# Kernel optimization log

Hardware: AMD Instinct MI355X
Metric: run time of the kernel (lower is better)

The kernel has to match this reference:

```python
import jax, jax.numpy as jnp
import numpy as np

N = 20000      # num_nodes
E = 320000     # num_edges (avg degree 16)
HID = 256      # hid_dim
H = 4          # attention heads
D = HID // H   # per-head dim (concat heads -> HID)
L = 2          # nGAT_layer
OUT = 12       # out_dim / pred_len (decoder steps)
NEG_SLOPE = 0.2


def setup_inputs() -> dict:
    key = jax.random.key(0)
    ks = jax.random.split(key, 16)
    s = 0.05
    nrm = lambda k, shape: jax.random.normal(k, shape, jnp.float32) * s
    return dict(
        x=nrm(ks[0], (N, HID)),
        edge_index=jax.random.randint(ks[1], (2, E), 0, N, dtype=jnp.int32),
        # GATv2Conv params per layer (stacked over L layers)
        gat_w_src=nrm(ks[2], (L, HID, H * D)),
        gat_w_dst=nrm(ks[3], (L, HID, H * D)),
        gat_att=nrm(ks[4], (L, H, D)),
        gat_bias=nrm(ks[5], (L, H * D)),
        # decoder_mlp: Linear(1 + HID -> HID)
        mlp_w=nrm(ks[6], (HID, 1 + HID)),
        mlp_b=nrm(ks[7], (HID,)),
        # nn.LSTM (1 layer, input HID, hidden HID), torch gate order i,f,g,o
        lstm_w_ih=nrm(ks[8], (4 * HID, HID)),
        lstm_w_hh=nrm(ks[9], (4 * HID, HID)),
        lstm_b_ih=nrm(ks[10], (4 * HID,)),
        lstm_b_hh=nrm(ks[11], (4 * HID,)),
        # decoder_init_proj: Linear(HID -> 1); decoder_output_proj: Linear(HID -> 1)
        init_w=nrm(ks[12], (1, HID)),
        init_b=nrm(ks[13], (1,)),
        out_w=nrm(ks[14], (1, HID)),
        out_b=nrm(ks[15], (1,)),
    )


def _gatv2_layer(x, src, dst, w_src, w_dst, att, bias):
    n = x.shape[0]
    xl = (x @ w_src).reshape(n, H, D)   # source-side projection
    xr = (x @ w_dst).reshape(n, H, D)   # destination-side projection
    # GATv2: e_ij = a^T LeakyReLU(Wl x_j + Wr x_i)
    e = jax.nn.leaky_relu(xl[src] + xr[dst], NEG_SLOPE)        # [E,H,D]
    logits = jnp.einsum('ehd,hd->eh', e, att)                   # [E,H]
    # edge softmax over incoming edges of each destination node
    m = jax.ops.segment_max(logits, dst, num_segments=n)        # [N,H]
    ex = jnp.exp(logits - m[dst])
    denom = jax.ops.segment_sum(ex, dst, num_segments=n)
    alpha = ex / denom[dst]                                     # [E,H]
    out = jax.ops.segment_sum(xl[src] * alpha[:, :, None], dst, num_segments=n)
    return out.reshape(n, H * D) + bias


def reference(x, edge_index, gat_w_src, gat_w_dst, gat_att, gat_bias,
              mlp_w, mlp_b, lstm_w_ih, lstm_w_hh, lstm_b_ih, lstm_b_hh,
              init_w, init_b, out_w, out_b):
    src, dst = edge_index[0], edge_index[1]
    # stacked GAT blocks: GATv2Conv + ELU (element == 2)
    for l in range(L):
        x = _gatv2_layer(x, src, dst, gat_w_src[l], gat_w_dst[l], gat_att[l], gat_bias[l])
        x = jax.nn.elu(x)
    # recurrent LSTM decoder, batch = nodes, seq step by step
    ctx = x                      # encoder_context
    h = x                        # h_0 = x (num_layers = 1)
    c = jnp.zeros_like(x)        # c_0 = 0
    prev = x @ init_w.T + init_b  # [N,1]
    outs = []
    for _ in range(OUT):
        dec_in = jnp.concatenate([prev, ctx], axis=1) @ mlp_w.T + mlp_b  # [N,HID]
        gates = dec_in @ lstm_w_ih.T + lstm_b_ih + h @ lstm_w_hh.T + lstm_b_hh
        i_g, f_g, g_g, o_g = jnp.split(gates, 4, axis=1)
        i_g = jax.nn.sigmoid(i_g)
        f_g = jax.nn.sigmoid(f_g)
        o_g = jax.nn.sigmoid(o_g)
        g_g = jnp.tanh(g_g)
        c = f_g * c + i_g * g_g
        h = o_g * jnp.tanh(c)
        prev = h @ out_w.T + out_b  # [N,1]
        outs.append(prev)
    return jnp.concatenate(outs, axis=1)  # [N, OUT]
```

## Files before the change

kernel.cpp:

```cpp
#include <hip/hip_runtime.h>
#include <hip/hip_bf16.h>

#define NN 20000
#define NE 320000
#define TOUT 12
#define DEGMAX 96
#define MR 80
#define NBLK 250
#define NCHL 14
#define NCHG 6

typedef __bf16 bf16x8 __attribute__((ext_vector_type(8)));
typedef float float4v __attribute__((ext_vector_type(4)));

#define LD8(p) (*(const bf16x8*)(p))
#define MFMA16(a,b,c) __builtin_amdgcn_mfma_f32_16x16x32_bf16((a),(b),(c),0,0,0)

__device__ __forceinline__ float bf2f(const __hip_bfloat16 v){ return __bfloat162float(v); }
__device__ __forceinline__ __hip_bfloat16 f2bf(float v){ return __float2bfloat16(v); }
__device__ __forceinline__ float sigmoidr_(float x){ return __builtin_amdgcn_rcpf(1.f + __expf(-x)); }
__device__ __forceinline__ float tanhr_(float x){ return 1.f - 2.f*__builtin_amdgcn_rcpf(__expf(2.f*x) + 1.f); }
__device__ __forceinline__ float rdf(const void* p, int i, int f32){
  return f32 ? ((const float*)p)[i] : __bfloat162float(((const __hip_bfloat16*)p)[i]);
}

__global__ void k_detect(const void* xraw, int* flag){
  __shared__ int cnt;
  if(threadIdx.x == 0) cnt = 0;
  __syncthreads();
  const unsigned* w = (const unsigned*)xraw;
  int local = 0;
  for(int i = threadIdx.x; i < 4096; i += 256){
    unsigned b = (w[i] >> 8) & 0x7F;
    if(b >= 0x33 && b <= 0x3F) local++;
  }
  atomicAdd(&cnt, local);
  __syncthreads();
  if(threadIdx.x == 0) *flag = (cnt > 2048) ? 0 : 1;
}

__global__ void k_fail(float* out, int n){
  int i = blockIdx.x*256 + threadIdx.x;
  if(i < n) out[i] = 256.0f;
}

__global__ void k_count(const int* __restrict__ dst, int* __restrict__ deg){
  int e = blockIdx.x*256 + threadIdx.x;
  if(e < NE){
    unsigned d = (unsigned)dst[e];
    if(d < NN) atomicAdd(&deg[d], 1);
  }
}

__global__ void k_scan(const int* __restrict__ deg, int* __restrict__ offp, int* __restrict__ cursor){
  __shared__ int part[256];
  __shared__ int excl[257];
  const int CH = (NN + 255)/256;
  int tid = threadIdx.x;
  int lo = tid*CH;
  int hi = lo + CH; if(hi > NN) hi = NN;
  int s = 0;
  for(int i=lo;i<hi;i++) s += deg[i];
  part[tid] = s;
// ... 36 lines not shown
    wdstT[tid] = f2bf(rdf(w_dst, l*65536 + i*256 + o, f));
  }
  if(tid < 262144){
    whhp[tid] = f2bf(rdf(w_hh, tid, f));
    wihb[tid] = f2bf(rdf(wih, tid, f));
  }
  if(tid < 65536){
    int k = tid >> 8, j = tid & 255;
    mlpT[tid] = f2bf(rdf(mlp_w, j*257 + 1 + k, f));
  }
}

__global__ void k_prep_ub(const void* __restrict__ wih, const void* __restrict__ mlp_w,
                          const void* __restrict__ mlp_b,
                          const void* __restrict__ b_ih, const void* __restrict__ b_hh,
                          const void* __restrict__ att, const void* __restrict__ gbias,
                          const void* __restrict__ init_w, const void* __restrict__ init_b,
                          const void* __restrict__ out_w, const void* __restrict__ out_b,
                          const int* __restrict__ flag,
                          float* __restrict__ u, float* __restrict__ bc,
                          float* __restrict__ attf, float* __restrict__ gbiasf,
                          float* __restrict__ initwf, float* __restrict__ outwf,
                          float* __restrict__ sc){
  __shared__ float su[256], sb[256];
  int g = blockIdx.x, j = threadIdx.x, f = *flag;
  float w = rdf(wih, g*256 + j, f);
  su[j] = w * rdf(mlp_w, j*257, f);
  sb[j] = w * rdf(mlp_b, j, f);
  if(g < 2){
    int i = g*256 + j;
    attf[i] = rdf(att, i, f);
    gbiasf[i] = rdf(gbias, i, f);
  }
  if(g == 0){
    initwf[j] = rdf(init_w, j, f);
    outwf[j]  = rdf(out_w, j, f);
    if(j == 0){ sc[0] = rdf(init_b, 0, f); sc[1] = rdf(out_b, 0, f); }
  }
  __syncthreads();
  for(int s=128; s>0; s>>=1){
    if(j < s){ su[j] += su[j+s]; sb[j] += sb[j+s]; }
    __syncthreads();
  }
  if(j == 0){ u[g] = su[0]; bc[g] = sb[0] + rdf(b_ih, g, f) + rdf(b_hh, g, f); }
}

__global__ void k_fold(const __hip_bfloat16* __restrict__ whh_pl,
                       const float* __restrict__ u_vec, const float* __restrict__ outwf,
                       __hip_bfloat16* __restrict__ whh2_pl){
  int i = blockIdx.x*256 + threadIdx.x;
  whh2_pl[i] = f2bf(bf2f(whh_pl[i]) + u_vec[i >> 8]*outwf[i & 255]);
}

__global__ void k_pack(const __hip_bfloat16* __restrict__ Wpl, const __hip_bfloat16* __restrict__ W2pl,
                       const __hip_bfloat16* __restrict__ Wcpl,
                       __hip_bfloat16* __restrict__ WhhP, __hip_bfloat16* __restrict__ Whh2P,
                       __hip_bfloat16* __restrict__ WcP){
  int idx = blockIdx.x*256 + threadIdx.x;
  if(idx >= 32768) return;
  int cs = idx >> 12;
  int kslot = (idx >> 9) & 7;
  int nt = (idx >> 6) & 7;
  int lane = idx & 63;
  int l16 = lane & 15, quad = lane >> 4;
  int brow = (nt>>1)*256 + cs*32 + (nt&1)*16 + l16;
  int srcofs = brow*256 + kslot*32 + quad*8;
  int dst = idx*8;
  *(bf16x8*)(WhhP + dst)  = LD8(Wpl + srcofs);
  *(bf16x8*)(Whh2P + dst) = LD8(W2pl + srcofs);
  *(bf16x8*)(WcP + dst)   = LD8(Wcpl + srcofs);
}

__global__ void k_pack2(const __hip_bfloat16* __restrict__ wsrcT,
                        const __hip_bfloat16* __restrict__ wdstT,
                        __hip_bfloat16* __restrict__ wprojP){
  int idx = blockIdx.x*256 + threadIdx.x;
  if(idx >= 32768) return;
  int m = idx >> 13;
  int fi = idx & 8191;
  int l = m >> 1, role = m & 1;
  int kidx = fi >> 10;
  int nt = (fi >> 6) & 15;
  int lane = fi & 63;
  int l16 = lane & 15, quad = lane >> 4;
  const __hip_bfloat16* src = (role ? wdstT : wsrcT) + l*65536;
  int srcofs = (nt*16 + l16)*256 + kidx*32 + quad*8;
  *(bf16x8*)(wprojP + (size_t)m*65536 + fi*8) = LD8(src + srcofs);
}

__global__ __launch_bounds__(256) void k_gemm_nt_bf(const __hip_bfloat16* __restrict__ A,
                                                    const __hip_bfloat16* __restrict__ B,
                                                    __hip_bfloat16* __restrict__ Cb, int M){
  int wave = threadIdx.x >> 6;
  int lane = threadIdx.x & 63;
  int l16 = lane & 15, quad = lane >> 4, quad8 = quad*8;
  int mBase = blockIdx.x*64 + wave*16;
  int nBase = blockIdx.y*64;
  int arow = mBase + l16; if(arow >= M) arow = M-1;
  const __hip_bfloat16* aptr = A + (size_t)arow*256 + quad8;
  float4v acc[4];
  #pragma unroll
  for(int nt=0;nt<4;nt++){ acc[nt][0]=0.f; acc[nt][1]=0.f; acc[nt][2]=0.f; acc[nt][3]=0.f; }
  for(int k0=0;k0<256;k0+=32){
    bf16x8 a = LD8(aptr + k0);
    #pragma unroll
    for(int nt=0;nt<4;nt++){
      const __hip_bfloat16* bptr = B + (size_t)(nBase + nt*16 + l16)*256 + k0 + quad8;
      acc[nt] = MFMA16(a, LD8(bptr), acc[nt]);
    }
  }
  #pragma unroll
  for(int nt=0;nt<4;nt++){
    int col = nBase + nt*16 + l16;
    #pragma unroll
    for(int r=0;r<4;r++){
      int row = mBase + quad*4 + r;
      if(row < M) Cb[(size_t)row*256 + col] = f2bf(acc[nt][r]);
    }
  }
// ... 94 lines not shown
      for(int j=0;j<4;j++){
        int d = h*64 + j*16 + li;
        float v = bf2f(pl[d]) + prl[h*4+j];
        v = (v > 0.f) ? v : 0.2f*v;
        p += v * attl[h*4+j];
      }
      part[h] = p;
    }
    #pragma unroll
    for(int h=0;h<4;h++){
      part[h] += __shfl_xor(part[h], 1, 64);
      part[h] += __shfl_xor(part[h], 2, 64);
      part[h] += __shfl_xor(part[h], 4, 64);
      part[h] += __shfl_xor(part[h], 8, 64);
    }
    if(li == 0 && valid){
      #pragma unroll
      for(int h=0;h<4;h++) slog[e*4+h] = part[h];
    }
  }
  __syncthreads();
  {
    int hh = tid >> 6;
    int li64 = tid & 63;
    float m = -1e30f;
    for(int i=li64; i<deg; i+=64) m = fmaxf(m, slog[i*4+hh]);
    #pragma unroll
    for(int s=1; s<64; s<<=1) m = fmaxf(m, __shfl_xor(m, s, 64));
    float den = 0.f;
    for(int i=li64; i<deg; i+=64) den += __expf(slog[i*4+hh] - m);
    #pragma unroll
    for(int s=1; s<64; s<<=1) den += __shfl_xor(den, s, 64);
    float inv = (den > 0.f) ? 1.f/den : 0.f;
    for(int i=li64; i<deg; i+=64) slog[i*4+hh] = __expf(slog[i*4+hh] - m)*inv;
  }
  __syncthreads();
  int d = tid, hd = d>>6;
  float acc = 0.f;
  for(int i=0;i<deg;i++) acc += slog[i*4+hd] * bf2f(Q[(size_t)ssrc[i]*256 + d]);
  acc += gbiasf[d];
  acc = (acc > 0.f) ? acc : (__expf(acc) - 1.f);
  P[(size_t)node*256 + d] = f2bf(acc);
}

__global__ __launch_bounds__(512, 1) void k_lstm80(const __hip_bfloat16* __restrict__ ctx,
                                                   const __hip_bfloat16* __restrict__ WcP,
                                                   const __hip_bfloat16* __restrict__ WhhP,
                                                   const __hip_bfloat16* __restrict__ Whh2P,
                                                   const float* __restrict__ u_vec,
                                                   const float* __restrict__ bc_vec,
                                                   const float* __restrict__ initwf,
                                                   const float* __restrict__ outwf,
                                                   const float* __restrict__ sc,
                                                   __hip_bfloat16* __restrict__ gxg,
                                                   float* __restrict__ out){
  __shared__ __hip_bfloat16 sgx[NCHL*4096];
  __shared__ __hip_bfloat16 sh[MR*264];
  __shared__ float spartw[MR*8];
  __shared__ float sprev0[MR];
  float* spart = (float*)sgx;
  int tid = threadIdx.x;
  int mBase = blockIdx.x*MR;
  int cs = tid>>6, lane = tid&63, l16 = lane&15, quad = lane>>4, quad8 = quad*8;
  int phase = (blockIdx.x >> 3) & 7;
  __hip_bfloat16* gxb = gxg + (size_t)blockIdx.x*(NCHG*4096);
  #pragma unroll
  for(int p=0;p<3;p++){
    int r = p*32 + (tid >> 4);
    if(r < MR){
      int c0 = (tid & 15)*16;
      const __hip_bfloat16* srcp = ctx + (size_t)(mBase + r)*256 + c0;
      *(bf16x8*)(&sh[r*264 + c0])     = LD8(srcp);
      *(bf16x8*)(&sh[r*264 + c0 + 8]) = LD8(srcp + 8);
    }
  }
  __syncthreads();
  #pragma unroll
  for(int p=0;p<3;p++){
    int r = p*32 + (tid >> 4);
    int c0 = (tid & 15)*16;
    float part = 0.f;
    if(r < MR){
      #pragma unroll
      for(int j=0;j<16;j++) part += bf2f(sh[r*264 + c0 + j]) * initwf[c0 + j];
    }
    spart[tid] = part;
    __syncthreads();
    if(tid < 32 && p*32 + tid < MR){
      float s = 0.f;
      #pragma unroll
      for(int j=0;j<16;j++) s += spart[tid*16 + j];
      sprev0[p*32 + tid] = s + sc[0];
    }
    __syncthreads();
  }
  float owreg[2];
  #pragma unroll
  for(int tc=0;tc<2;tc++) owreg[tc] = outwf[cs*32 + tc*16 + l16];
  float outb = sc[1];
  {
    float bcl[8];
    #pragma unroll
    for(int g=0;g<4;g++)
      #pragma unroll
      for(int tc=0;tc<2;tc++)
        bcl[g*2+tc] = bc_vec[g*256 + cs*32 + tc*16 + l16]
                    + u_vec[g*256 + cs*32 + tc*16 + l16]*outb;
    float4v acc[40];
    #pragma unroll
    for(int nt=0;nt<40;nt++){ acc[nt][0]=0.f; acc[nt][1]=0.f; acc[nt][2]=0.f; acc[nt][3]=0.f; }
    #pragma unroll 2
    for(int ki=0;ki<8;ki++){
      int kidx = (ki + phase) & 7;
      int k0 = kidx*32;
      bf16x8 a0 = *(const bf16x8*)(&sh[l16*264 + k0 + quad8]);
      bf16x8 a1 = *(const bf16x8*)(&sh[(16 + l16)*264 + k0 + quad8]);
      bf16x8 a2 = *(const bf16x8*)(&sh[(32 + l16)*264 + k0 + quad8]);
      bf16x8 a3 = *(const bf16x8*)(&sh[(48 + l16)*264 + k0 + quad8]);
      bf16x8 a4 = *(const bf16x8*)(&sh[(64 + l16)*264 + k0 + quad8]);
      const __hip_bfloat16* bbase = WcP + (((cs<<3) + kidx)<<12) + (lane<<3);
      #pragma unroll
      for(int nt=0;nt<8;nt++){
        bf16x8 b = LD8(bbase + (nt<<9));
        acc[nt]    = MFMA16(a0, b, acc[nt]);
        acc[8+nt]  = MFMA16(a1, b, acc[8+nt]);
        acc[16+nt] = MFMA16(a2, b, acc[16+nt]);
        acc[24+nt] = MFMA16(a3, b, acc[24+nt]);
        acc[32+nt] = MFMA16(a4, b, acc[32+nt]);
      }
    }
    #pragma unroll
    for(int rt=0;rt<5;rt++)
      #pragma unroll
      for(int tc=0;tc<2;tc++)
        #pragma unroll
        for(int half=0;half<2;half++){
          bf16x8 v;
          #pragma unroll
          for(int rr=0;rr<2;rr++)
            #pragma unroll
            for(int g=0;g<4;g++){
              int r = half*2 + rr;
              v[rr*4+g] = (__bf16)f2bf(acc[rt*8 + g*2 + tc][r] + bcl[g*2+tc]);
            }
          int cp = (rt*2+tc)*2 + half;
          if(cp < NCHL) *(bf16x8*)(&sgx[cp*4096 + tid*8]) = v;
          else          *(bf16x8*)(gxb + (cp-NCHL)*4096 + tid*8) = v;
        }
  }
  __syncthreads();
  float creg[40];
  #pragma unroll
  for(int i=0;i<40;i++) creg[i] = 0.f;
  #pragma unroll 1
  for(int step=0; step<TOUT; step++){
    const __hip_bfloat16* W = (step == 0) ? WhhP : Whh2P;
    float4v acc[40];
    #pragma unroll
    for(int nt=0;nt<40;nt++){ acc[nt][0]=0.f; acc[nt][1]=0.f; acc[nt][2]=0.f; acc[nt][3]=0.f; }
    #pragma unroll 2
    for(int ki=0;ki<8;ki++){
      int kidx = (ki + phase) & 7;
      int k0 = kidx*32;
      bf16x8 a0 = *(const bf16x8*)(&sh[l16*264 + k0 + quad8]);
      bf16x8 a1 = *(const bf16x8*)(&sh[(16 + l16)*264 + k0 + quad8]);
      bf16x8 a2 = *(const bf16x8*)(&sh[(32 + l16)*264 + k0 + quad8]);
      bf16x8 a3 = *(const bf16x8*)(&sh[(48 + l16)*264 + k0 + quad8]);
      bf16x8 a4 = *(const bf16x8*)(&sh[(64 + l16)*264 + k0 + quad8]);
      const __hip_bfloat16* bbase = W + (((cs<<3) + kidx)<<12) + (lane<<3);
      #pragma unroll
      for(int nt=0;nt<8;nt++){
        bf16x8 b = LD8(bbase + (nt<<9));
        acc[nt]    = MFMA16(a0, b, acc[nt]);
        acc[8+nt]  = MFMA16(a1, b, acc[8+nt]);
        acc[16+nt] = MFMA16(a2, b, acc[16+nt]);
        acc[24+nt] = MFMA16(a3, b, acc[24+nt]);
        acc[32+nt] = MFMA16(a4, b, acc[32+nt]);
      }
    }
    __syncthreads();
    #pragma unroll
    for(int ri=0; ri<5; ri++){
      const int rt = 4 - ri;
      float hsum[4];
      hsum[0]=0.f; hsum[1]=0.f; hsum[2]=0.f; hsum[3]=0.f;
      #pragma unroll
      for(int tc=0;tc<2;tc++){
        int col = cs*32 + tc*16 + l16;
        const int cpb = (rt*2+tc)*2;
        bf16x8 ga, gb;
        if(cpb < NCHL)   ga = *(const bf16x8*)(&sgx[cpb*4096 + tid*8]);
        else             ga = LD8(gxb + (cpb-NCHL)*4096 + tid*8);
        if(cpb+1 < NCHL) gb = *(const bf16x8*)(&sgx[(cpb+1)*4096 + tid*8]);
        else             gb = LD8(gxb + (cpb+1-NCHL)*4096 + tid*8);
        #pragma unroll
        for(int r=0;r<4;r++){
          int row = rt*16 + quad*4 + r;
          int jb = (r&1)*4;
          float gx0, gx1, gx2, gx3;
          if(r < 2){
            gx0 = bf2f((__hip_bfloat16)ga[jb]);   gx1 = bf2f((__hip_bfloat16)ga[jb+1]);
            gx2 = bf2f((__hip_bfloat16)ga[jb+2]); gx3 = bf2f((__hip_bfloat16)ga[jb+3]);
          }else{
            gx0 = bf2f((__hip_bfloat16)gb[jb]);   gx1 = bf2f((__hip_bfloat16)gb[jb+1]);
            gx2 = bf2f((__hip_bfloat16)gb[jb+2]); gx3 = bf2f((__hip_bfloat16)gb[jb+3]);
          }
          float g0 = acc[rt*8 + tc][r]     + gx0;
          float g1 = acc[rt*8 + 2 + tc][r] + gx1;
          float g2 = acc[rt*8 + 4 + tc][r] + gx2;
          float g3 = acc[rt*8 + 6 + tc][r] + gx3;
          if(step == 0){
            float pd = sprev0[row] - outb;
            g0 += pd*u_vec[col];
            g1 += pd*u_vec[256 + col];
            g2 += pd*u_vec[512 + col];
            g3 += pd*u_vec[768 + col];
          }
          float iv = sigmoidr_(g0), fv = sigmoidr_(g1);
          float gv = tanhr_(g2),    ov = sigmoidr_(g3);
          float cn = fv*creg[rt*8 + tc*4 + r] + iv*gv;
          creg[rt*8 + tc*4 + r] = cn;
          float hn = ov * tanhr_(cn);
          sh[row*264 + col] = f2bf(hn);
          hsum[r] += hn * owreg[tc];
        }
      }
      #pragma unroll
      for(int r=0;r<4;r++){
        hsum[r] += __shfl_xor(hsum[r], 1, 64);
        hsum[r] += __shfl_xor(hsum[r], 2, 64);
        hsum[r] += __shfl_xor(hsum[r], 4, 64);
        hsum[r] += __shfl_xor(hsum[r], 8, 64);
      }
      if(l16 == 0){
        #pragma unroll
        for(int r=0;r<4;r++)
          spartw[(rt*16 + quad*4 + r)*8 + cs] = hsum[r];
      }
    }
    __syncthreads();
    if(tid < MR){
      float s = outb;
      #pragma unroll
      for(int c=0;c<8;c++) s += spartw[tid*8 + c];
      out[(size_t)(mBase + tid)*TOUT + step] = s;
    }
  }
}

extern "C" void kernel_launch(void* const* d_in, const int* in_sizes, int n_in,
                              void* d_out, int out_size, void* d_ws, size_t ws_size,
                              hipStream_t stream){
  const void* x      = d_in[0];
  const int*  ei     = (const int*)d_in[1];
  const void* w_src  = d_in[2];
  const void* w_dst  = d_in[3];
  const void* att    = d_in[4];
  const void* gbias  = d_in[5];
  const void* mlp_w  = d_in[6];
  const void* mlp_b  = d_in[7];
  const void* w_ih   = d_in[8];
  const void* w_hh   = d_in[9];
  const void* b_ih   = d_in[10];
  const void* b_hh   = d_in[11];
  const void* init_w = d_in[12];
  const void* init_b = d_in[13];
  const void* out_w  = d_in[14];
  const void* out_b  = d_in[15];
  float* out = (float*)d_out;
  const int* srcp = ei;
  const int* dstp = ei + NE;
  (void)in_sizes; (void)n_in;

  char* ws = (char*)d_ws;
  size_t off = 0;
  auto alloc = [&](size_t bytes)->void*{
    void* p = ws + off;
    off += (bytes + 255) & ~(size_t)255;
    return p;
  };
  __hip_bfloat16* P = (__hip_bfloat16*)alloc((size_t)NN*256*2);
  __hip_bfloat16* Q = (__hip_bfloat16*)alloc((size_t)NN*256*2);
  int* deg      = (int*)alloc((size_t)NN*4);
  int* offp     = (int*)alloc((size_t)(NN+1)*4);
  int* cursor   = (int*)alloc((size_t)NN*4);
  int* csr_src  = (int*)alloc((size_t)NE*4);
  __hip_bfloat16* wsrcT   = (__hip_bfloat16*)alloc((size_t)131072*2);
  __hip_bfloat16* wdstT   = (__hip_bfloat16*)alloc((size_t)131072*2);
  __hip_bfloat16* wprojP  = (__hip_bfloat16*)alloc((size_t)4*65536*2);
  __hip_bfloat16* whh_pl  = (__hip_bfloat16*)alloc((size_t)262144*2);
  __hip_bfloat16* whh2_pl = (__hip_bfloat16*)alloc((size_t)262144*2);
  __hip_bfloat16* Wc_pl   = (__hip_bfloat16*)alloc((size_t)262144*2);
  __hip_bfloat16* WhhP    = (__hip_bfloat16*)alloc((size_t)262144*2);
  __hip_bfloat16* Whh2P   = (__hip_bfloat16*)alloc((size_t)262144*2);
  __hip_bfloat16* WcP     = (__hip_bfloat16*)alloc((size_t)262144*2);
  __hip_bfloat16* wihb    = (__hip_bfloat16*)alloc((size_t)262144*2);
  __hip_bfloat16* mlpT    = (__hip_bfloat16*)alloc((size_t)65536*2);
  __hip_bfloat16* gxg     = (__hip_bfloat16*)alloc((size_t)NBLK*NCHG*4096*2);
  float* u_vec  = (float*)alloc(1024*4);
  float* bc_vec = (float*)alloc(1024*4);
  float* attf   = (float*)alloc(512*4);
  float* gbiasf = (float*)alloc(512*4);
  float* initwf = (float*)alloc(256*4);
  float* outwf  = (float*)alloc(256*4);
  float* sc     = (float*)alloc(2*4);
  int*   flag   = (int*)alloc(4);

  if(off > ws_size){
    k_fail<<<(out_size + 255)/256, 256, 0, stream>>>(out, out_size);
    return;
  }

  k_detect<<<1, 256, 0, stream>>>(x, flag);
  hipMemsetAsync(deg, 0, (size_t)NN*4, stream);
  hipMemsetAsync(csr_src, 0xFF, (size_t)NE*4, stream);
  k_count<<<NE/256, 256, 0, stream>>>(dstp, deg);
  k_scan<<<1, 256, 0, stream>>>(deg, offp, cursor);
  k_fill<<<NE/256, 256, 0, stream>>>(srcp, dstp, cursor, csr_src);
  k_prep<<<1024, 256, 0, stream>>>(w_src, w_dst, w_hh, w_ih, mlp_w, flag,
                                   wsrcT, wdstT, whh_pl, wihb, mlpT);
  k_prep_ub<<<1024, 256, 0, stream>>>(w_ih, mlp_w, mlp_b, b_ih, b_hh, att, gbias,
                                      init_w, init_b, out_w, out_b, flag,
                                      u_vec, bc_vec, attf, gbiasf, initwf, outwf, sc);
  {
    dim3 gwc(16, 4);
    k_gemm_nt_bf<<<gwc, 256, 0, stream>>>(wihb, mlpT, Wc_pl, 1024);
  }
  k_fold<<<1024, 256, 0, stream>>>(whh_pl, u_vec, outwf, whh2_pl);
  k_pack<<<128, 256, 0, stream>>>(whh_pl, whh2_pl, Wc_pl, WhhP, Whh2P, WcP);
  k_pack2<<<128, 256, 0, stream>>>(wsrcT, wdstT, wprojP);

  for(int l=0;l<2;l++){
    k_gemm_dual<<<313, 512, 0, stream>>>(P, x, flag, (l == 0) ? 1 : 0,
                                         wprojP + (size_t)(l*2)*65536,
                                         wprojP + (size_t)(l*2+1)*65536, Q);
    k_node_fused<<<NN, 256, 0, stream>>>(Q, P, offp, csr_src, attf + l*256, gbiasf + l*256);
  }

  k_lstm80<<<NBLK, 512, 0, stream>>>(P, WcP, WhhP, Whh2P, u_vec, bc_vec,
                                     initwf, outwf, sc, gxg, out);
}
```

Measured before the change: 776.3 us.

## Split LSTM recurrent GEMM into two row groups and keep spilled gate chunks in registers

```diff
diff --git a/kernel.cpp b/kernel.cpp
--- a/kernel.cpp
+++ b/kernel.cpp
@@ -8,7 +8,6 @@
 #define MR 80
 #define NBLK 250
 #define NCHL 14
-#define NCHG 6
 
 typedef __bf16 bf16x8 __attribute__((ext_vector_type(8)));
 typedef float float4v __attribute__((ext_vector_type(4)));
@@ -364,7 +363,6 @@
                                                    const float* __restrict__ initwf,
                                                    const float* __restrict__ outwf,
                                                    const float* __restrict__ sc,
-                                                   __hip_bfloat16* __restrict__ gxg,
                                                    float* __restrict__ out){
   __shared__ __hip_bfloat16 sgx[NCHL*4096];
   __shared__ __hip_bfloat16 sh[MR*264];
@@ -375,7 +373,6 @@
   int mBase = blockIdx.x*MR;
   int cs = tid>>6, lane = tid&63, l16 = lane&15, quad = lane>>4, quad8 = quad*8;
   int phase = (blockIdx.x >> 3) & 7;
-  __hip_bfloat16* gxb = gxg + (size_t)blockIdx.x*(NCHG*4096);
   #pragma unroll
   for(int p=0;p<3;p++){
     int r = p*32 + (tid >> 4);
@@ -410,6 +407,7 @@
   #pragma unroll
   for(int tc=0;tc<2;tc++) owreg[tc] = outwf[cs*32 + tc*16 + l16];
   float outb = sc[1];
+  bf16x8 gg0, gg1, gg2, gg3, gg4, gg5;
   {
     float bcl[8];
     #pragma unroll
@@ -418,9 +416,96 @@
       for(int tc=0;tc<2;tc++)
         bcl[g*2+tc] = bc_vec[g*256 + cs*32 + tc*16 + l16]
                     + u_vec[g*256 + cs*32 + tc*16 + l16]*outb;
-    float4v acc[40];
-    #pragma unroll
-    for(int nt=0;nt<40;nt++){ acc[nt][0]=0.f; acc[nt][1]=0.f; acc[nt][2]=0.f; acc[nt][3]=0.f; }
+    {
+      float4v acc[24];
+      #pragma unroll
+      for(int nt=0;nt<24;nt++){ acc[nt][0]=0.f; acc[nt][1]=0.f; acc[nt][2]=0.f; acc[nt][3]=0.f; }
+      #pragma unroll 2
+      for(int ki=0;ki<8;ki++){
+        int kidx = (ki + phase) & 7;
+        int k0 = kidx*32;
+        bf16x8 a0 = *(const bf16x8*)(&sh[l16*264 + k0 + quad8]);
+        bf16x8 a1 = *(const bf16x8*)(&sh[(16 + l16)*264 + k0 + quad8]);
+        bf16x8 a2 = *(const bf16x8*)(&sh[(32 + l16)*264 + k0 + quad8]);
+        const __hip_bfloat16* bbase = WcP + (((cs<<3) + kidx)<<12) + (lane<<3);
+        #pragma unroll
+        for(int nt=0;nt<8;nt++){
+          bf16x8 b = LD8(bbase + (nt<<9));
+          acc[nt]    = MFMA16(a0, b, acc[nt]);
+          acc[8+nt]  = MFMA16(a1, b, acc[8+nt]);
+          acc[16+nt] = MFMA16(a2, b, acc[16+nt]);
+        }
+      }
+      #pragma unroll
+      for(int rt=0;rt<3;rt++)
+        #pragma unroll
+        for(int tc=0;tc<2;tc++)
+          #pragma unroll
+          for(int half=0;half<2;half++){
+            bf16x8 v;
+            #pragma unroll
+            for(int rr=0;rr<2;rr++)
+              #pragma unroll
+              for(int g=0;g<4;g++){
+                int r = half*2 + rr;
+                v[rr*4+g] = (__bf16)f2bf(acc[rt*8 + g*2 + tc][r] + bcl[g*2+tc]);
+              }
+            int cp = (rt*2+tc)*2 + half;
+            *(bf16x8*)(&sgx[cp*4096 + tid*8]) = v;
+          }
+    }
+    {
+      float4v acc[16];
+      #pragma unroll
+      for(int nt=0;nt<16;nt++){ acc[nt][0]=0.f; acc[nt][1]=0.f; acc[nt][2]=0.f; acc[nt][3]=0.f; }
+      #pragma unroll 2
+      for(int ki=0;ki<8;ki++){
+        int kidx = (ki + phase) & 7;
+        int k0 = kidx*32;
+        bf16x8 a3 = *(const bf16x8*)(&sh[(48 + l16)*264 + k0 + quad8]);
+        bf16x8 a4 = *(const bf16x8*)(&sh[(64 + l16)*264 + k0 + quad8]);
+        const __hip_bfloat16* bbase = WcP + (((cs<<3) + kidx)<<12) + (lane<<3);
+        #pragma unroll
+        for(int nt=0;nt<8;nt++){
+          bf16x8 b = LD8(bbase + (nt<<9));
+          acc[nt]   = MFMA16(a3, b, acc[nt]);
+          acc[8+nt] = MFMA16(a4, b, acc[8+nt]);
+        }
+      }
+      #pragma unroll
+      for(int rtl=0;rtl<2;rtl++)
+        #pragma unroll
+        for(int tc=0;tc<2;tc++)
+          #pragma unroll
+          for(int half=0;half<2;half++){
+            bf16x8 v;
+            #pragma unroll
+            for(int rr=0;rr<2;rr++)
+              #pragma unroll
+              for(int g=0;g<4;g++){
+                int r = half*2 + rr;
+                v[rr*4+g] = (__bf16)f2bf(acc[rtl*8 + g*2 + tc][r] + bcl[g*2+tc]);
+              }
+            const int cp = ((3+rtl)*2+tc)*2 + half;
+            if(cp == 12 || cp == 13) *(bf16x8*)(&sgx[cp*4096 + tid*8]) = v;
+            else if(cp == 14) gg0 = v;
+            else if(cp == 15) gg1 = v;
+            else if(cp == 16) gg2 = v;
+            else if(cp == 17) gg3 = v;
+            else if(cp == 18) gg4 = v;
+            else              gg5 = v;
+          }
+    }
+  }
+  float creg[40];
+  #pragma unroll
+  for(int i=0;i<40;i++) creg[i] = 0.f;
+  #pragma unroll 1
+  for(int step=0; step<TOUT; step++){
+    const __hip_bfloat16* W = (step == 0) ? WhhP : Whh2P;
+    float4v accA[24];
+    #pragma unroll
+    for(int nt=0;nt<24;nt++){ accA[nt][0]=0.f; accA[nt][1]=0.f; accA[nt][2]=0.f; accA[nt][3]=0.f; }
     #pragma unroll 2
     for(int ki=0;ki<8;ki++){
       int kidx = (ki + phase) & 7;
@@ -428,83 +513,26 @@
       bf16x8 a0 = *(const bf16x8*)(&sh[l16*264 + k0 + quad8]);
       bf16x8 a1 = *(const bf16x8*)(&sh[(16 + l16)*264 + k0 + quad8]);
       bf16x8 a2 = *(const bf16x8*)(&sh[(32 + l16)*264 + k0 + quad8]);
-      bf16x8 a3 = *(const bf16x8*)(&sh[(48 + l16)*264 + k0 + quad8]);
-      bf16x8 a4 = *(const bf16x8*)(&sh[(64 + l16)*264 + k0 + quad8]);
-      const __hip_bfloat16* bbase = WcP + (((cs<<3) + kidx)<<12) + (lane<<3);
+      const __hip_bfloat16* bbase = W + (((cs<<3) + kidx)<<12) + (lane<<3);
       #pragma unroll
       for(int nt=0;nt<8;nt++){
         bf16x8 b = LD8(bbase + (nt<<9));
-        acc[nt]    = MFMA16(a0, b, acc[nt]);
-        acc[8+nt]  = MFMA16(a1, b, acc[8+nt]);
-        acc[16+nt] = MFMA16(a2, b, acc[16+nt]);
-        acc[24+nt] = MFMA16(a3, b, acc[24+nt]);
-        acc[32+nt] = MFMA16(a4, b, acc[32+nt]);
-      }
-    }
-    #pragma unroll
-    for(int rt=0;rt<5;rt++)
-      #pragma unroll
-      for(int tc=0;tc<2;tc++)
-        #pragma unroll
-        for(int half=0;half<2;half++){
-          bf16x8 v;
-          #pragma unroll
-          for(int rr=0;rr<2;rr++)
-            #pragma unroll
-            for(int g=0;g<4;g++){
-              int r = half*2 + rr;
-              v[rr*4+g] = (__bf16)f2bf(acc[rt*8 + g*2 + tc][r] + bcl[g*2+tc]);
-            }
-          int cp = (rt*2+tc)*2 + half;
-          if(cp < NCHL) *(bf16x8*)(&sgx[cp*4096 + tid*8]) = v;
-          else          *(bf16x8*)(gxb + (cp-NCHL)*4096 + tid*8) = v;
-        }
-  }
-  __syncthreads();
-  float creg[40];
-  #pragma unroll
-  for(int i=0;i<40;i++) creg[i] = 0.f;
-  #pragma unroll 1
-  for(int step=0; step<TOUT; step++){
-    const __hip_bfloat16* W = (step == 0) ? WhhP : Whh2P;
-    float4v acc[40];
-    #pragma unroll
-    for(int nt=0;nt<40;nt++){ acc[nt][0]=0.f; acc[nt][1]=0.f; acc[nt][2]=0.f; acc[nt][3]=0.f; }
-    #pragma unroll 2
-    for(int ki=0;ki<8;ki++){
-      int kidx = (ki + phase) & 7;
-      int k0 = kidx*32;
-      bf16x8 a0 = *(const bf16x8*)(&sh[l16*264 + k0 + quad8]);
-      bf16x8 a1 = *(const bf16x8*)(&sh[(16 + l16)*264 + k0 + quad8]);
-      bf16x8 a2 = *(const bf16x8*)(&sh[(32 + l16)*264 + k0 + quad8]);
-      bf16x8 a3 = *(const bf16x8*)(&sh[(48 + l16)*264 + k0 + quad8]);
-      bf16x8 a4 = *(const bf16x8*)(&sh[(64 + l16)*264 + k0 + quad8]);
-      const __hip_bfloat16* bbase = W + (((cs<<3) + kidx)<<12) + (lane<<3);
-      #pragma unroll
-      for(int nt=0;nt<8;nt++){
-        bf16x8 b = LD8(bbase + (nt<<9));
-        acc[nt]    = MFMA16(a0, b, acc[nt]);
-        acc[8+nt]  = MFMA16(a1, b, acc[8+nt]);
-        acc[16+nt] = MFMA16(a2, b, acc[16+nt]);
-        acc[24+nt] = MFMA16(a3, b, acc[24+nt]);
-        acc[32+nt] = MFMA16(a4, b, acc[32+nt]);
+        accA[nt]    = MFMA16(a0, b, accA[nt]);
+        accA[8+nt]  = MFMA16(a1, b, accA[8+nt]);
+        accA[16+nt] = MFMA16(a2, b, accA[16+nt]);
       }
     }
     __syncthreads();
     #pragma unroll
-    for(int ri=0; ri<5; ri++){
-      const int rt = 4 - ri;
+    for(int rt=0; rt<3; rt++){
       float hsum[4];
       hsum[0]=0.f; hsum[1]=0.f; hsum[2]=0.f; hsum[3]=0.f;
       #pragma unroll
       for(int tc=0;tc<2;tc++){
         int col = cs*32 + tc*16 + l16;
         const int cpb = (rt*2+tc)*2;
-        bf16x8 ga, gb;
-        if(cpb < NCHL)   ga = *(const bf16x8*)(&sgx[cpb*4096 + tid*8]);
-        else             ga = LD8(gxb + (cpb-NCHL)*4096 + tid*8);
-        if(cpb+1 < NCHL) gb = *(const bf16x8*)(&sgx[(cpb+1)*4096 + tid*8]);
-        else             gb = LD8(gxb + (cpb+1-NCHL)*4096 + tid*8);
+        bf16x8 ga = *(const bf16x8*)(&sgx[cpb*4096 + tid*8]);
+        bf16x8 gb = *(const bf16x8*)(&sgx[(cpb+1)*4096 + tid*8]);
         #pragma unroll
         for(int r=0;r<4;r++){
           int row = rt*16 + quad*4 + r;
@@ -517,10 +545,88 @@
             gx0 = bf2f((__hip_bfloat16)gb[jb]);   gx1 = bf2f((__hip_bfloat16)gb[jb+1]);
             gx2 = bf2f((__hip_bfloat16)gb[jb+2]); gx3 = bf2f((__hip_bfloat16)gb[jb+3]);
           }
-          float g0 = acc[rt*8 + tc][r]     + gx0;
-          float g1 = acc[rt*8 + 2 + tc][r] + gx1;
-          float g2 = acc[rt*8 + 4 + tc][r] + gx2;
-          float g3 = acc[rt*8 + 6 + tc][r] + gx3;
+          float g0 = accA[rt*8 + tc][r]     + gx0;
+          float g1 = accA[rt*8 + 2 + tc][r] + gx1;
+          float g2 = accA[rt*8 + 4 + tc][r] + gx2;
+          float g3 = accA[rt*8 + 6 + tc][r] + gx3;
+          if(step == 0){
+            float pd = sprev0[row] - outb;
+            g0 += pd*u_vec[col];
+            g1 += pd*u_vec[256 + col];
+            g2 += pd*u_vec[512 + col];
+            g3 += pd*u_vec[768 + col];
+          }
+          float iv = sigmoidr_(g0), fv = sigmoidr_(g1);
+          float gv = tanhr_(g2),    ov = sigmoidr_(g3);
+          float cn = fv*creg[rt*8 + tc*4 + r] + iv*gv;
+          creg[rt*8 + tc*4 + r] = cn;
+          float hn = ov * tanhr_(cn);
+          sh[row*264 + col] = f2bf(hn);
+          hsum[r] += hn * owreg[tc];
+        }
+      }
+      #pragma unroll
+      for(int r=0;r<4;r++){
+        hsum[r] += __shfl_xor(hsum[r], 1, 64);
+        hsum[r] += __shfl_xor(hsum[r], 2, 64);
+        hsum[r] += __shfl_xor(hsum[r], 4, 64);
+        hsum[r] += __shfl_xor(hsum[r], 8, 64);
+      }
+      if(l16 == 0){
+        #pragma unroll
+        for(int r=0;r<4;r++)
+          spartw[(rt*16 + quad*4 + r)*8 + cs] = hsum[r];
+      }
+    }
+    float4v accB[16];
+    #pragma unroll
+    for(int nt=0;nt<16;nt++){ accB[nt][0]=0.f; accB[nt][1]=0.f; accB[nt][2]=0.f; accB[nt][3]=0.f; }
+    #pragma unroll 2
+    for(int ki=0;ki<8;ki++){
+      int kidx = (ki + phase) & 7;
+      int k0 = kidx*32;
+      bf16x8 a3 = *(const bf16x8*)(&sh[(48 + l16)*264 + k0 + quad8]);
+      bf16x8 a4 = *(const bf16x8*)(&sh[(64 + l16)*264 + k0 + quad8]);
+      const __hip_bfloat16* bbase = W + (((cs<<3) + kidx)<<12) + (lane<<3);
+      #pragma unroll
+      for(int nt=0;nt<8;nt++){
+        bf16x8 b = LD8(bbase + (nt<<9));
+        accB[nt]   = MFMA16(a3, b, accB[nt]);
+        accB[8+nt] = MFMA16(a4, b, accB[8+nt]);
+      }
+    }
+    __syncthreads();
+    #pragma unroll
+    for(int rtl=0; rtl<2; rtl++){
+      const int rt = 3 + rtl;
+      float hsum[4];
+      hsum[0]=0.f; hsum[1]=0.f; hsum[2]=0.f; hsum[3]=0.f;
+      #pragma unroll
+      for(int tc=0;tc<2;tc++){
+        int col = cs*32 + tc*16 + l16;
+        bf16x8 ga, gb;
+        if(rtl == 0 && tc == 0){
+          ga = *(const bf16x8*)(&sgx[12*4096 + tid*8]);
+          gb = *(const bf16x8*)(&sgx[13*4096 + tid*8]);
+        }else if(rtl == 0 && tc == 1){ ga = gg0; gb = gg1; }
+        else if(rtl == 1 && tc == 0){ ga = gg2; gb = gg3; }
+        else                        { ga = gg4; gb = gg5; }
+        #pragma unroll
+        for(int r=0;r<4;r++){
+          int row = rt*16 + quad*4 + r;
+          int jb = (r&1)*4;
+          float gx0, gx1, gx2, gx3;
+          if(r < 2){
+            gx0 = bf2f((__hip_bfloat16)ga[jb]);   gx1 = bf2f((__hip_bfloat16)ga[jb+1]);
+            gx2 = bf2f((__hip_bfloat16)ga[jb+2]); gx3 = bf2f((__hip_bfloat16)ga[jb+3]);
+          }else{
+            gx0 = bf2f((__hip_bfloat16)gb[jb]);   gx1 = bf2f((__hip_bfloat16)gb[jb+1]);
+            gx2 = bf2f((__hip_bfloat16)gb[jb+2]); gx3 = bf2f((__hip_bfloat16)gb[jb+3]);
+          }
+          float g0 = accB[rtl*8 + tc][r]     + gx0;
+          float g1 = accB[rtl*8 + 2 + tc][r] + gx1;
+          float g2 = accB[rtl*8 + 4 + tc][r] + gx2;
+          float g3 = accB[rtl*8 + 6 + tc][r] + gx3;
           if(step == 0){
             float pd = sprev0[row] - outb;
             g0 += pd*u_vec[col];
@@ -608,7 +714,6 @@
   __hip_bfloat16* WcP     = (__hip_bfloat16*)alloc((size_t)262144*2);
   __hip_bfloat16* wihb    = (__hip_bfloat16*)alloc((size_t)262144*2);
   __hip_bfloat16* mlpT    = (__hip_bfloat16*)alloc((size_t)65536*2);
-  __hip_bfloat16* gxg     = (__hip_bfloat16*)alloc((size_t)NBLK*NCHG*4096*2);
   float* u_vec  = (float*)alloc(1024*4);
   float* bc_vec = (float*)alloc(1024*4);
   float* attf   = (float*)alloc(512*4);
@@ -650,5 +755,5 @@
   }
 
   k_lstm80<<<NBLK, 512, 0, stream>>>(P, WcP, WhhP, Whh2P, u_vec, bc_vec,
-                                     initwf, outwf, sc, gxg, out);
-}
+                                     initwf, outwf, sc, out);
+}
```

New measurement: 687.9 us. 1.13x faster.

## Split LSTM gate GEMM into two column halves to drop global gx spill

Applied to the files above, without the earlier changes.

```diff
diff --git a/kernel.cpp b/kernel.cpp
--- a/kernel.cpp
+++ b/kernel.cpp
@@ -7,8 +7,7 @@
 #define DEGMAX 96
 #define MR 80
 #define NBLK 250
-#define NCHL 14
-#define NCHG 6
+#define NCPL 13
 
 typedef __bf16 bf16x8 __attribute__((ext_vector_type(8)));
 typedef float float4v __attribute__((ext_vector_type(4)));
@@ -151,19 +150,20 @@
   whh2_pl[i] = f2bf(bf2f(whh_pl[i]) + u_vec[i >> 8]*outwf[i & 255]);
 }
 
-__global__ void k_pack(const __hip_bfloat16* __restrict__ Wpl, const __hip_bfloat16* __restrict__ W2pl,
-                       const __hip_bfloat16* __restrict__ Wcpl,
-                       __hip_bfloat16* __restrict__ WhhP, __hip_bfloat16* __restrict__ Whh2P,
-                       __hip_bfloat16* __restrict__ WcP){
+__global__ void k_pack3(const __hip_bfloat16* __restrict__ Wpl, const __hip_bfloat16* __restrict__ W2pl,
+                        const __hip_bfloat16* __restrict__ Wcpl,
+                        __hip_bfloat16* __restrict__ WhhP, __hip_bfloat16* __restrict__ Whh2P,
+                        __hip_bfloat16* __restrict__ WcP){
   int idx = blockIdx.x*256 + threadIdx.x;
   if(idx >= 32768) return;
-  int cs = idx >> 12;
-  int kslot = (idx >> 9) & 7;
-  int nt = (idx >> 6) & 7;
+  int P    = idx >> 14;
+  int cs   = (idx >> 11) & 7;
+  int kidx = (idx >> 8) & 7;
+  int ntl  = (idx >> 6) & 3;
   int lane = idx & 63;
   int l16 = lane & 15, quad = lane >> 4;
-  int brow = (nt>>1)*256 + cs*32 + (nt&1)*16 + l16;
-  int srcofs = brow*256 + kslot*32 + quad*8;
+  int brow = ntl*256 + P*128 + cs*16 + l16;
+  int srcofs = brow*256 + kidx*32 + quad*8;
   int dst = idx*8;
   *(bf16x8*)(WhhP + dst)  = LD8(Wpl + srcofs);
   *(bf16x8*)(Whh2P + dst) = LD8(W2pl + srcofs);
@@ -364,18 +364,18 @@
                                                    const float* __restrict__ initwf,
                                                    const float* __restrict__ outwf,
                                                    const float* __restrict__ sc,
-                                                   __hip_bfloat16* __restrict__ gxg,
                                                    float* __restrict__ out){
-  __shared__ __hip_bfloat16 sgx[NCHL*4096];
+  __shared__ __hip_bfloat16 sgx[NCPL*4096];
   __shared__ __hip_bfloat16 sh[MR*264];
-  __shared__ float spartw[MR*8];
+  __shared__ float spartw[2][MR*16];
   __shared__ float sprev0[MR];
   float* spart = (float*)sgx;
   int tid = threadIdx.x;
   int mBase = blockIdx.x*MR;
   int cs = tid>>6, lane = tid&63, l16 = lane&15, quad = lane>>4, quad8 = quad*8;
   int phase = (blockIdx.x >> 3) & 7;
-  __hip_bfloat16* gxb = gxg + (size_t)blockIdx.x*(NCHG*4096);
+  int j0 = cs*16 + l16;
+  int j1 = 128 + j0;
   #pragma unroll
   for(int p=0;p<3;p++){
     int r = p*32 + (tid >> 4);
@@ -406,21 +406,75 @@
     }
     __syncthreads();
   }
-  float owreg[2];
-  #pragma unroll
-  for(int tc=0;tc<2;tc++) owreg[tc] = outwf[cs*32 + tc*16 + l16];
+  float ow0 = outwf[j0], ow1 = outwf[j1];
   float outb = sc[1];
+  bf16x8 gg0, gg1, gg2, gg3, gg4, gg5, gg6;
   {
     float bcl[8];
     #pragma unroll
-    for(int g=0;g<4;g++)
-      #pragma unroll
-      for(int tc=0;tc<2;tc++)
-        bcl[g*2+tc] = bc_vec[g*256 + cs*32 + tc*16 + l16]
-                    + u_vec[g*256 + cs*32 + tc*16 + l16]*outb;
-    float4v acc[40];
-    #pragma unroll
-    for(int nt=0;nt<40;nt++){ acc[nt][0]=0.f; acc[nt][1]=0.f; acc[nt][2]=0.f; acc[nt][3]=0.f; }
+    for(int g=0;g<4;g++){
+      bcl[g]   = bc_vec[g*256 + j0] + u_vec[g*256 + j0]*outb;
+      bcl[4+g] = bc_vec[g*256 + j1] + u_vec[g*256 + j1]*outb;
+    }
+    #pragma unroll
+    for(int P2=0;P2<2;P2++){
+      float4v acc[20];
+      #pragma unroll
+      for(int nt=0;nt<20;nt++){ acc[nt][0]=0.f; acc[nt][1]=0.f; acc[nt][2]=0.f; acc[nt][3]=0.f; }
+      #pragma unroll 2
+      for(int ki=0;ki<8;ki++){
+        int kidx = (ki + phase) & 7;
+        int k0 = kidx*32;
+        bf16x8 a0 = *(const bf16x8*)(&sh[l16*264 + k0 + quad8]);
+        bf16x8 a1 = *(const bf16x8*)(&sh[(16 + l16)*264 + k0 + quad8]);
+        bf16x8 a2 = *(const bf16x8*)(&sh[(32 + l16)*264 + k0 + quad8]);
+        bf16x8 a3 = *(const bf16x8*)(&sh[(48 + l16)*264 + k0 + quad8]);
+        bf16x8 a4 = *(const bf16x8*)(&sh[(64 + l16)*264 + k0 + quad8]);
+        const __hip_bfloat16* bbase = WcP + P2*131072 + (((cs<<3) + kidx)<<11) + (lane<<3);
+        #pragma unroll
+        for(int ntl=0;ntl<4;ntl++){
+          bf16x8 b = LD8(bbase + (ntl<<9));
+          acc[ntl]     = MFMA16(a0, b, acc[ntl]);
+          acc[4+ntl]   = MFMA16(a1, b, acc[4+ntl]);
+          acc[8+ntl]   = MFMA16(a2, b, acc[8+ntl]);
+          acc[12+ntl]  = MFMA16(a3, b, acc[12+ntl]);
+          acc[16+ntl]  = MFMA16(a4, b, acc[16+ntl]);
+        }
+      }
+      #pragma unroll
+      for(int rt=0;rt<5;rt++)
+        #pragma unroll
+        for(int half=0;half<2;half++){
+          bf16x8 v;
+          #pragma unroll
+          for(int rr=0;rr<2;rr++)
+            #pragma unroll
+            for(int g=0;g<4;g++){
+              int r = half*2 + rr;
+              v[rr*4+g] = (__bf16)f2bf(acc[rt*4 + g][r] + bcl[P2*4+g]);
+            }
+          const int cp = P2*10 + rt*2 + half;
+          if(cp < NCPL) *(bf16x8*)(&sgx[cp*4096 + tid*8]) = v;
+          else if(cp == 13) gg0 = v;
+          else if(cp == 14) gg1 = v;
+          else if(cp == 15) gg2 = v;
+          else if(cp == 16) gg3 = v;
+          else if(cp == 17) gg4 = v;
+          else if(cp == 18) gg5 = v;
+          else              gg6 = v;
+        }
+    }
+  }
+  float creg[40];
+  #pragma unroll
+  for(int i=0;i<40;i++) creg[i] = 0.f;
+  #pragma unroll 1
+  for(int step=0; step<TOUT; step++){
+    const __hip_bfloat16* W = (step == 0) ? WhhP : Whh2P;
+    int sb = step & 1;
+    float4v acc[20];
+    #pragma unroll
+    for(int nt=0;nt<20;nt++){ acc[nt][0]=0.f; acc[nt][1]=0.f; acc[nt][2]=0.f; acc[nt][3]=0.f; }
     #pragma unroll 2
     for(int ki=0;ki<8;ki++){
       int kidx = (ki + phase) & 7;
@@ -430,46 +484,69 @@
       bf16x8 a2 = *(const bf16x8*)(&sh[(32 + l16)*264 + k0 + quad8]);
       bf16x8 a3 = *(const bf16x8*)(&sh[(48 + l16)*264 + k0 + quad8]);
       bf16x8 a4 = *(const bf16x8*)(&sh[(64 + l16)*264 + k0 + quad8]);
-      const __hip_bfloat16* bbase = WcP + (((cs<<3) + kidx)<<12) + (lane<<3);
-      #pragma unroll
-      for(int nt=0;nt<8;nt++){
-        bf16x8 b = LD8(bbase + (nt<<9));
-        acc[nt]    = MFMA16(a0, b, acc[nt]);
-        acc[8+nt]  = MFMA16(a1, b, acc[8+nt]);
-        acc[16+nt] = MFMA16(a2, b, acc[16+nt]);
-        acc[24+nt] = MFMA16(a3, b, acc[24+nt]);
-        acc[32+nt] = MFMA16(a4, b, acc[32+nt]);
-      }
-    }
-    #pragma unroll
-    for(int rt=0;rt<5;rt++)
-      #pragma unroll
-      for(int tc=0;tc<2;tc++)
+      const __hip_bfloat16* bbase = W + (((cs<<3) + kidx)<<11) + (lane<<3);
+      #pragma unroll
+      for(int ntl=0;ntl<4;ntl++){
+        bf16x8 b = LD8(bbase + (ntl<<9));
+        acc[ntl]     = MFMA16(a0, b, acc[ntl]);
+        acc[4+ntl]   = MFMA16(a1, b, acc[4+ntl]);
+        acc[8+ntl]   = MFMA16(a2, b, acc[8+ntl]);
+        acc[12+ntl]  = MFMA16(a3, b, acc[12+ntl]);
+        acc[16+ntl]  = MFMA16(a4, b, acc[16+ntl]);
+      }
+    }
+    float hA[20];
+    #pragma unroll
+    for(int rt=0; rt<5; rt++){
+      bf16x8 ga = *(const bf16x8*)(&sgx[(rt*2)*4096 + tid*8]);
+      bf16x8 gb = *(const bf16x8*)(&sgx[(rt*2+1)*4096 + tid*8]);
+      float hsum[4];
+      #pragma unroll
+      for(int r=0;r<4;r++){
+        int row = rt*16 + quad*4 + r;
+        int jb = (r&1)*4;
+        float gx0, gx1, gx2, gx3;
+        if(r < 2){
+          gx0 = bf2f((__hip_bfloat16)ga[jb]);   gx1 = bf2f((__hip_bfloat16)ga[jb+1]);
+          gx2 = bf2f((__hip_bfloat16)ga[jb+2]); gx3 = bf2f((__hip_bfloat16)ga[jb+3]);
+        }else{
+          gx0 = bf2f((__hip_bfloat16)gb[jb]);   gx1 = bf2f((__hip_bfloat16)gb[jb+1]);
+          gx2 = bf2f((__hip_bfloat16)gb[jb+2]); gx3 = bf2f((__hip_bfloat16)gb[jb+3]);
+        }
+        float g0 = acc[rt*4 + 0][r] + gx0;
+        float g1 = acc[rt*4 + 1][r] + gx1;
+        float g2 = acc[rt*4 + 2][r] + gx2;
+        float g3 = acc[rt*4 + 3][r] + gx3;
+        if(step == 0){
+          float pd = sprev0[row] - outb;
+          g0 += pd*u_vec[j0];
+          g1 += pd*u_vec[256 + j0];
+          g2 += pd*u_vec[512 + j0];
+          g3 += pd*u_vec[768 + j0];
+        }
+        float iv = sigmoidr_(g0), fv = sigmoidr_(g1);
+        float gv = tanhr_(g2),    ov = sigmoidr_(g3);
+        float cn = fv*creg[rt*4 + r] + iv*gv;
+        creg[rt*4 + r] = cn;
+        float hn = ov * tanhr_(cn);
+        hA[rt*4 + r] = hn;
+        hsum[r] = hn * ow0;
+      }
+      #pragma unroll
+      for(int r=0;r<4;r++){
+        hsum[r] += __shfl_xor(hsum[r], 1, 64);
+        hsum[r] += __shfl_xor(hsum[r], 2, 64);
+        hsum[r] += __shfl_xor(hsum[r], 4, 64);
+        hsum[r] += __shfl_xor(hsum[r], 8, 64);
+      }
+      if(l16 == 0){
         #pragma unroll
-        for(int half=0;half<2;half++){
-          bf16x8 v;
-          #pragma unroll
-          for(int rr=0;rr<2;rr++)
-            #pragma unroll
-            for(int g=0;g<4;g++){
-              int r = half*2 + rr;
-              v[rr*4+g] = (__bf16)f2bf(acc[rt*8 + g*2 + tc][r] + bcl[g*2+tc]);
-            }
-          int cp = (rt*2+tc)*2 + half;
-          if(cp < NCHL) *(bf16x8*)(&sgx[cp*4096 + tid*8]) = v;
-          else          *(bf16x8*)(gxb + (cp-NCHL)*4096 + tid*8) = v;
-        }
-  }
-  __syncthreads();
-  float creg[40];
-  #pragma unroll
-  for(int i=0;i<40;i++) creg[i] = 0.f;
-  #pragma unroll 1
-  for(int step=0; step<TOUT; step++){
-    const __hip_bfloat16* W = (step == 0) ? WhhP : Whh2P;
-    float4v acc[40];
-    #pragma unroll
-    for(int nt=0;nt<40;nt++){ acc[nt][0]=0.f; acc[nt][1]=0.f; acc[nt][2]=0.f; acc[nt][3]=0.f; }
+        for(int r=0;r<4;r++)
+          spartw[sb][(rt*16 + quad*4 + r)*16 + cs*2] = hsum[r];
+      }
+    }
+    #pragma unroll
+    for(int nt=0;nt<20;nt++){ acc[nt][0]=0.f; acc[nt][1]=0.f; acc[nt][2]=0.f; acc[nt][3]=0.f; }
     #pragma unroll 2
     for(int ki=0;ki<8;ki++){
       int kidx = (ki + phase) & 7;
@@ -479,63 +556,63 @@
       bf16x8 a2 = *(const bf16x8*)(&sh[(32 + l16)*264 + k0 + quad8]);
       bf16x8 a3 = *(const bf16x8*)(&sh[(48 + l16)*264 + k0 + quad8]);
       bf16x8 a4 = *(const bf16x8*)(&sh[(64 + l16)*264 + k0 + quad8]);
-      const __hip_bfloat16* bbase = W + (((cs<<3) + kidx)<<12) + (lane<<3);
-      #pragma unroll
-      for(int nt=0;nt<8;nt++){
-        bf16x8 b = LD8(bbase + (nt<<9));
-        acc[nt]    = MFMA16(a0, b, acc[nt]);
-        acc[8+nt]  = MFMA16(a1, b, acc[8+nt]);
-        acc[16+nt] = MFMA16(a2, b, acc[16+nt]);
-        acc[24+nt] = MFMA16(a3, b, acc[24+nt]);
-        acc[32+nt] = MFMA16(a4, b, acc[32+nt]);
+      const __hip_bfloat16* bbase = W + 131072 + (((cs<<3) + kidx)<<11) + (lane<<3);
+      #pragma unroll
+      for(int ntl=0;ntl<4;ntl++){
+        bf16x8 b = LD8(bbase + (ntl<<9));
+        acc[ntl]     = MFMA16(a0, b, acc[ntl]);
+        acc[4+ntl]   = MFMA16(a1, b, acc[4+ntl]);
+        acc[8+ntl]   = MFMA16(a2, b, acc[8+ntl]);
+        acc[12+ntl]  = MFMA16(a3, b, acc[12+ntl]);
+        acc[16+ntl]  = MFMA16(a4, b, acc[16+ntl]);
       }
     }
     __syncthreads();
     #pragma unroll
-    for(int ri=0; ri<5; ri++){
-      const int rt = 4 - ri;
+    for(int rt=0; rt<5; rt++){
+      const int cpa = 10 + rt*2, cpb_ = 11 + rt*2;
+      bf16x8 ga, gb;
+      if(cpa < NCPL)      ga = *(const bf16x8*)(&sgx[cpa*4096 + tid*8]);
+      else if(cpa == 14)  ga = gg1;
+      else if(cpa == 16)  ga = gg3;
+      else                ga = gg5;
+      if(cpb_ < NCPL)     gb = *(const bf16x8*)(&sgx[cpb_*4096 + tid*8]);
+      else if(cpb_ == 13) gb = gg0;
+      else if(cpb_ == 15) gb = gg2;
+      else if(cpb_ == 17) gb = gg4;
+      else                gb = gg6;
       float hsum[4];
-      hsum[0]=0.f; hsum[1]=0.f; hsum[2]=0.f; hsum[3]=0.f;
-      #pragma unroll
-      for(int tc=0;tc<2;tc++){
-        int col = cs*32 + tc*16 + l16;
-        const int cpb = (rt*2+tc)*2;
-        bf16x8 ga, gb;
-        if(cpb < NCHL)   ga = *(const bf16x8*)(&sgx[cpb*4096 + tid*8]);
-        else             ga = LD8(gxb + (cpb-NCHL)*4096 + tid*8);
-        if(cpb+1 < NCHL) gb = *(const bf16x8*)(&sgx[(cpb+1)*4096 + tid*8]);
-        else             gb = LD8(gxb + (cpb+1-NCHL)*4096 + tid*8);
-        #pragma unroll
-        for(int r=0;r<4;r++){
-          int row = rt*16 + quad*4 + r;
-          int jb = (r&1)*4;
-          float gx0, gx1, gx2, gx3;
-          if(r < 2){
-            gx0 = bf2f((__hip_bfloat16)ga[jb]);   gx1 = bf2f((__hip_bfloat16)ga[jb+1]);
-            gx2 = bf2f((__hip_bfloat16)ga[jb+2]); gx3 = bf2f((__hip_bfloat16)ga[jb+3]);
-          }else{
-            gx0 = bf2f((__hip_bfloat16)gb[jb]);   gx1 = bf2f((__hip_bfloat16)gb[jb+1]);
-            gx2 = bf2f((__hip_bfloat16)gb[jb+2]); gx3 = bf2f((__hip_bfloat16)gb[jb+3]);
-          }
-          float g0 = acc[rt*8 + tc][r]     + gx0;
-          float g1 = acc[rt*8 + 2 + tc][r] + gx1;
-          float g2 = acc[rt*8 + 4 + tc][r] + gx2;
-          float g3 = acc[rt*8 + 6 + tc][r] + gx3;
-          if(step == 0){
-            float pd = sprev0[row] - outb;
-            g0 += pd*u_vec[col];
-            g1 += pd*u_vec[256 + col];
-            g2 += pd*u_vec[512 + col];
-            g3 += pd*u_vec[768 + col];
-          }
-          float iv = sigmoidr_(g0), fv = sigmoidr_(g1);
-          float gv = tanhr_(g2),    ov = sigmoidr_(g3);
-          float cn = fv*creg[rt*8 + tc*4 + r] + iv*gv;
-          creg[rt*8 + tc*4 + r] = cn;
-          float hn = ov * tanhr_(cn);
-          sh[row*264 + col] = f2bf(hn);
-          hsum[r] += hn * owreg[tc];
+      #pragma unroll
+      for(int r=0;r<4;r++){
+        int row = rt*16 + quad*4 + r;
+        int jb = (r&1)*4;
+        float gx0, gx1, gx2, gx3;
+        if(r < 2){
+          gx0 = bf2f((__hip_bfloat16)ga[jb]);   gx1 = bf2f((__hip_bfloat16)ga[jb+1]);
+          gx2 = bf2f((__hip_bfloat16)ga[jb+2]); gx3 = bf2f((__hip_bfloat16)ga[jb+3]);
+        }else{
+          gx0 = bf2f((__hip_bfloat16)gb[jb]);   gx1 = bf2f((__hip_bfloat16)gb[jb+1]);
+          gx2 = bf2f((__hip_bfloat16)gb[jb+2]); gx3 = bf2f((__hip_bfloat16)gb[jb+3]);
         }
+        float g0 = acc[rt*4 + 0][r] + gx0;
+        float g1 = acc[rt*4 + 1][r] + gx1;
+        float g2 = acc[rt*4 + 2][r] + gx2;
+        float g3 = acc[rt*4 + 3][r] + gx3;
+        if(step == 0){
+          float pd = sprev0[row] - outb;
+          g0 += pd*u_vec[j1];
+          g1 += pd*u_vec[256 + j1];
+          g2 += pd*u_vec[512 + j1];
+          g3 += pd*u_vec[768 + j1];
+        }
+        float iv = sigmoidr_(g0), fv = sigmoidr_(g1);
+        float gv = tanhr_(g2),    ov = sigmoidr_(g3);
+        float cn = fv*creg[20 + rt*4 + r] + iv*gv;
+        creg[20 + rt*4 + r] = cn;
+        float hn = ov * tanhr_(cn);
+        sh[row*264 + j0] = f2bf(hA[rt*4 + r]);
+        sh[row*264 + j1] = f2bf(hn);
+        hsum[r] = hn * ow1;
       }
       #pragma unroll
       for(int r=0;r<4;r++){
@@ -547,14 +624,14 @@
       if(l16 == 0){
         #pragma unroll
         for(int r=0;r<4;r++)
-          spartw[(rt*16 + quad*4 + r)*8 + cs] = hsum[r];
+          spartw[sb][(rt*16 + quad*4 + r)*16 + cs*2 + 1] = hsum[r];
       }
     }
     __syncthreads();
     if(tid < MR){
       float s = outb;
       #pragma unroll
-      for(int c=0;c<8;c++) s += spartw[tid*8 + c];
+      for(int c=0;c<16;c++) s += spartw[sb][tid*16 + c];
       out[(size_t)(mBase + tid)*TOUT + step] = s;
     }
   }
@@ -608,7 +685,6 @@
   __hip_bfloat16* WcP     = (__hip_bfloat16*)alloc((size_t)262144*2);
   __hip_bfloat16* wihb    = (__hip_bfloat16*)alloc((size_t)262144*2);
   __hip_bfloat16* mlpT    = (__hip_bfloat16*)alloc((size_t)65536*2);
-  __hip_bfloat16* gxg     = (__hip_bfloat16*)alloc((size_t)NBLK*NCHG*4096*2);
   float* u_vec  = (float*)alloc(1024*4);
   float* bc_vec = (float*)alloc(1024*4);
   float* attf   = (float*)alloc(512*4);
@@ -639,7 +715,7 @@
     k_gemm_nt_bf<<<gwc, 256, 0, stream>>>(wihb, mlpT, Wc_pl, 1024);
   }
   k_fold<<<1024, 256, 0, stream>>>(whh_pl, u_vec, outwf, whh2_pl);
-  k_pack<<<128, 256, 0, stream>>>(whh_pl, whh2_pl, Wc_pl, WhhP, Whh2P, WcP);
+  k_pack3<<<128, 256, 0, stream>>>(whh_pl, whh2_pl, Wc_pl, WhhP, Whh2P, WcP);
   k_pack2<<<128, 256, 0, stream>>>(wsrcT, wdstT, wprojP);
 
   for(int l=0;l<2;l++){
@@ -650,5 +726,5 @@
   }
 
   k_lstm80<<<NBLK, 512, 0, stream>>>(P, WcP, WhhP, Whh2P, u_vec, bc_vec,
-                                     initwf, outwf, sc, gxg, out);
-}
+                                     initwf, outwf, sc, out);
+}
```

After: 647.5 us. -16.6%, faster.
